# Kernel tuning notes

Hardware: AMD Instinct MI355X
Metric: run time of the kernel (lower is better)

## Reference

```python
import jax, jax.numpy as jnp
import numpy as np

H = 256       # hidden_dim
E = H // 2    # operator embedding dim
T = 12        # num_tempers
O = 3         # num_ops per temper
HOPS = 4      # max_path_hops
B = 128       # batch
D = 2048      # input_dim
NCLS = 10     # task_head classes


def setup_inputs() -> dict:
    key = jax.random.key(0)
    ks = jax.random.split(key, 12)
    x = jax.random.normal(ks[0], (B, D), jnp.float32)
    N = B * (D // H)  # 1024 patch tokens
    # per-hop routed temper per patch; value == T means halt
    sampled_tempers = jax.random.randint(ks[1], (HOPS, N), 0, T + 1, jnp.int32)
    sampled_ops = jax.random.randint(ks[2], (HOPS, N), 0, O, jnp.int32)
    s1 = 1.0 / np.sqrt(H + E)
    W1 = jax.random.uniform(ks[3], (T, O, H + E, H), jnp.float32, -s1, s1)
    b1 = jax.random.uniform(ks[4], (T, O, H), jnp.float32, -s1, s1)
    s2 = 1.0 / np.sqrt(H)
    W2 = jax.random.uniform(ks[5], (T, O, H, H), jnp.float32, -s2, s2)
    b2 = jax.random.uniform(ks[6], (T, O, H), jnp.float32, -s2, s2)
    op_emb = jax.random.normal(ks[7], (T, O, E), jnp.float32)
    ln_g = jnp.ones((H,), jnp.float32)
    ln_b = jnp.zeros((H,), jnp.float32)
    Wt = jax.random.uniform(ks[8], (H, NCLS), jnp.float32, -s2, s2)
    bt = jax.random.uniform(ks[9], (NCLS,), jnp.float32, -s2, s2)
    return dict(x=x, W1=W1, b1=b1, W2=W2, b2=b2, op_emb=op_emb,
                ln_g=ln_g, ln_b=ln_b, Wt=Wt, bt=bt,
                sampled_tempers=sampled_tempers, sampled_ops=sampled_ops)


def reference(x, W1, b1, W2, b2, op_emb, ln_g, ln_b, Wt, bt,
              sampled_tempers, sampled_ops):
    Bsz, Din = x.shape
    pad = (-Din) % H
    if pad > 0:
        x = jnp.pad(x, ((0, 0), (0, pad)))
    state = x.reshape(-1, H)                       # [N, H] patch states
    active = jnp.ones((state.shape[0],), bool)     # not-yet-halted mask
    for hop in range(HOPS):
        t = sampled_tempers[hop]
        o = sampled_ops[hop]
        active = active & (t != T)                 # T == halt action
        tc = jnp.clip(t, 0, T - 1)                 # safe index for halted rows
        emb = op_emb[tc, o]                        # [N, E] op embedding gather
        xa = jnp.concatenate([state, emb], axis=-1)  # [N, H+E]
        # per-token expert weight gather + batched matvec (memory-bound dispatch)
        h = jax.nn.relu(jnp.einsum('ni,nio->no', xa, W1[tc, o]) + b1[tc, o])
        y = jax.nn.relu(jnp.einsum('ni,nio->no', h, W2[tc, o]) + b2[tc, o])
        state = jnp.where(active[:, None], y, state)
    pooled = state.reshape(Bsz, -1, H).mean(axis=1)   # [B, H]
    mu = pooled.mean(axis=-1, keepdims=True)
    var = pooled.var(axis=-1, keepdims=True)
    normed = (pooled - mu) * jax.lax.rsqrt(var + 1e-5) * ln_g + ln_b
    return normed @ Wt + bt                           # [B, 10]
```

## Files before the change

### kernel.cpp

```cpp
#include <hip/hip_runtime.h>

typedef __attribute__((ext_vector_type(8))) short short8;
typedef __attribute__((ext_vector_type(4))) float floatx4;

#define NEXP   36
#define NTOK   1024
#define HOPS   4

#define OFF_STATE   0u
#define OFF_W1B     1048576u
#define OFF_W2B     5767168u
#define OFF_C1      10485760u
#define OFF_COUNTS  10522624u
#define OFF_LISTS   10523264u

__device__ __forceinline__ unsigned short f2bf(float f) {
    unsigned u = __float_as_uint(f);
    u += 0x7FFFu + ((u >> 16) & 1u);
    return (unsigned short)(u >> 16);
}

__global__ __launch_bounds__(256) void prep_kernel(
    const float* __restrict__ x, const float* __restrict__ W1,
    const float* __restrict__ b1, const float* __restrict__ W2,
    const float* __restrict__ op_emb,
    const int* __restrict__ tempers, const int* __restrict__ ops,
    float* __restrict__ state, unsigned short* __restrict__ W1b,
    unsigned short* __restrict__ W2b, float* __restrict__ c1,
    int* __restrict__ counts, int* __restrict__ lists)
{
    const int bid = blockIdx.x;
    const int t = threadIdx.x;

    if (bid < 2304) {
        const int mat = bid / 1152;
        const int id  = bid % 1152;
        const int e   = id / 32;
        const int sub = id % 32;
        const int kb  = sub / 4;
        const int jt  = sub % 4;
        const float* src = mat ? (W2 + e * 65536) : (W1 + e * 98304);
        unsigned short* dst = (mat ? W2b : W1b) + e * 65536;
        const int j  = jt * 64 + (t & 63);
        const int ks = (t >> 6) * 8;
        short8 v;
        #pragma unroll
        for (int i = 0; i < 8; i++)
            v[i] = (short)f2bf(src[(kb * 32 + ks + i) * 256 + j]);
        *(short8*)(dst + (kb * 256 + j) * 32 + ks) = v;
    } else if (bid < 2340) {
        const int e = bid - 2304;
        __shared__ float eb[128];
        if (t < 128) eb[t] = op_emb[e * 128 + t];
        __syncthreads();
        float acc = b1[e * 256 + t];
        const float* wp = W1 + e * 98304 + 256 * 256;
        #pragma unroll 4
        for (int k = 0; k < 128; k++)
            acc += eb[k] * wp[k * 256 + t];
        c1[e * 256 + t] = acc;
    } else if (bid < 2404) {
        const int cb = bid - 2340;
        const float4* xs = (const float4*)x;
        float4* ss = (float4*)state;
        #pragma unroll
        for (int p = 0; p < 4; p++) {
            int i4 = cb * 1024 + p * 256 + t;
            ss[i4] = xs[i4];
        }
    } else {
        __shared__ int lc[HOPS * NEXP];
        if (t < HOPS * NEXP) lc[t] = 0;
        __syncthreads();
        for (int q = 0; q < 4; q++) {
            int n = q * 256 + t;
            bool act = true;
            for (int hop = 0; hop < HOPS; hop++) {
                int tt = tempers[hop * NTOK + n];
                int oo = ops[hop * NTOK + n];
                act = act && (tt != 12);
                if (act) {
                    int e = tt * 3 + oo;
                    int pos = atomicAdd(&lc[hop * NEXP + e], 1);
                    lists[(hop * NEXP + e) * NTOK + pos] = n;
                }
            }
        }
        __syncthreads();
        if (t < HOPS * NEXP) counts[t] = lc[t];
    }
}

__global__ __launch_bounds__(1024) void hop_kernel(
    float* __restrict__ state,
    const unsigned short* __restrict__ W1b,
    const unsigned short* __restrict__ W2b,
    const float* __restrict__ c1, const float* __restrict__ b2,
    const int* __restrict__ counts, const int* __restrict__ lists, int hop)
{
    const int e   = blockIdx.x;
    const int n_e = counts[hop * NEXP + e];
    if (n_e == 0) return;

    const int t = threadIdx.x;
    const int l = t & 63, w = t >> 6;
    const int col = l & 15, g = l >> 4;
    const int j = w * 16 + col;

    const unsigned short* Wp  = W1b + e * 65536;
    const unsigned short* Wp2 = W2b + e * 65536;
    short8 B1[8], B2[8];
    #pragma unroll
    for (int kb = 0; kb < 8; kb++) {
        B1[kb] = *(const short8*)(Wp  + (kb * 256 + j) * 32 + g * 8);
        B2[kb] = *(const short8*)(Wp2 + (kb * 256 + j) * 32 + g * 8);
    }
    const float cv = c1[e * 256 + j];
    const float bv = b2[e * 256 + j];

    __shared__ int toks[16];
    __shared__ unsigned short Ab[4096];
    __shared__ unsigned short Hb[4096];

    const int* lp = lists + (hop * NEXP + e) * NTOK;

    for (int m0 = 0; m0 < n_e; m0 += 16) {
        const int mact = min(16, n_e - m0);
        __syncthreads();
        if (t < 16) toks[t] = (t < mact) ? lp[m0 + t] : 0;
        __syncthreads();

        {
            int m = t >> 6;
            int k = (t & 63) * 4;
            float4 v = make_float4(0.f, 0.f, 0.f, 0.f);
            if (m < mact) v = *(const float4*)(state + toks[m] * 256 + k);
            int kb = k >> 5, gg = (k >> 3) & 3, i = k & 7;
            unsigned short* d = Ab + kb * 512 + (gg * 16 + m) * 8 + i;
            d[0] = f2bf(v.x); d[1] = f2bf(v.y); d[2] = f2bf(v.z); d[3] = f2bf(v.w);
        }
        __syncthreads();

        floatx4 acc = (floatx4){cv, cv, cv, cv};
        #pragma unroll
        for (int kb = 0; kb < 8; kb++) {
            short8 a = *(const short8*)(Ab + kb * 512 + l * 8);
            acc = __builtin_amdgcn_mfma_f32_16x16x32_bf16(a, B1[kb], acc, 0, 0, 0);
        }
        {
            int kb2 = j >> 5, g2 = (j >> 3) & 3, i2 = j & 7;
            #pragma unroll
            for (int r = 0; r < 4; r++) {
                int m = g * 4 + r;
                float vv = acc[r];
                vv = vv > 0.f ? vv : 0.f;
                Hb[kb2 * 512 + (g2 * 16 + m) * 8 + i2] = f2bf(vv);
            }
        }
        __syncthreads();

        floatx4 acc2 = (floatx4){bv, bv, bv, bv};
        #pragma unroll
        for (int kb = 0; kb < 8; kb++) {
            short8 a = *(const short8*)(Hb + kb * 512 + l * 8);
            acc2 = __builtin_amdgcn_mfma_f32_16x16x32_bf16(a, B2[kb], acc2, 0, 0, 0);
        }
        #pragma unroll
        for (int r = 0; r < 4; r++) {
            int m = g * 4 + r;
            if (m < mact) {
                float vv = acc2[r];
                state[toks[m] * 256 + j] = vv > 0.f ? vv : 0.f;
            }
        }
    }
}

__global__ __launch_bounds__(256) void final_kernel(
    const float* __restrict__ state, const float* __restrict__ ln_g,
    const float* __restrict__ ln_b, const float* __restrict__ Wt,
    const float* __restrict__ bt, float* __restrict__ out)
{
    const int b = blockIdx.x, t = threadIdx.x;
    float s = 0.f;
    #pragma unroll
    for (int p = 0; p < 8; p++) s += state[(b * 8 + p) * 256 + t];
    s *= 0.125f;

    float v1 = s, v2 = s * s;
    #pragma unroll
    for (int off = 32; off; off >>= 1) {
        v1 += __shfl_down(v1, off);
        v2 += __shfl_down(v2, off);
    }
    __shared__ float red[8];
    __shared__ float stats[2];
    const int w = t >> 6, l = t & 63;
    if (l == 0) { red[w] = v1; red[4 + w] = v2; }
    __syncthreads();
    if (t == 0) {
        float su = red[0] + red[1] + red[2] + red[3];
        float sq = red[4] + red[5] + red[6] + red[7];
        float mu = su * (1.0f / 256.0f);
        float var = sq * (1.0f / 256.0f) - mu * mu;
        stats[0] = mu;
        stats[1] = rsqrtf(var + 1e-5f);
    }
    __syncthreads();
    float normed = (s - stats[0]) * stats[1] * ln_g[t] + ln_b[t];

    __shared__ float pr[40];
    #pragma unroll
    for (int c = 0; c < 10; c++) {
        float pv = normed * Wt[t * 10 + c];
        #pragma unroll
        for (int off = 32; off; off >>= 1) pv += __shfl_down(pv, off);
        if (l == 0) pr[w * 10 + c] = pv;
    }
    __syncthreads();
    if (t < 10)
        out[b * 10 + t] = pr[t] + pr[10 + t] + pr[20 + t] + pr[30 + t] + bt[t];
}

extern "C" void kernel_launch(void* const* d_in, const int* in_sizes, int n_in,
                              void* d_out, int out_size, void* d_ws, size_t ws_size,
                              hipStream_t stream)
{
    const float* x      = (const float*)d_in[0];
    const float* W1     = (const float*)d_in[1];
    const float* b1     = (const float*)d_in[2];
    const float* W2     = (const float*)d_in[3];
    const float* b2     = (const float*)d_in[4];
    const float* op_emb = (const float*)d_in[5];
    const float* ln_g   = (const float*)d_in[6];
    const float* ln_b   = (const float*)d_in[7];
    const float* Wt     = (const float*)d_in[8];
    const float* bt     = (const float*)d_in[9];
    const int* tempers  = (const int*)d_in[10];
    const int* ops      = (const int*)d_in[11];

    char* ws = (char*)d_ws;
    float* state          = (float*)(ws + OFF_STATE);
    unsigned short* W1b   = (unsigned short*)(ws + OFF_W1B);
    unsigned short* W2b   = (unsigned short*)(ws + OFF_W2B);
    float* c1             = (float*)(ws + OFF_C1);
    int* counts           = (int*)(ws + OFF_COUNTS);
    int* lists            = (int*)(ws + OFF_LISTS);
    float* out            = (float*)d_out;

    prep_kernel<<<2405, 256, 0, stream>>>(x, W1, b1, W2, op_emb, tempers, ops,
                                          state, W1b, W2b, c1, counts, lists);
    for (int hop = 0; hop < HOPS; hop++)
        hop_kernel<<<NEXP, 1024, 0, stream>>>(state, W1b, W2b, c1, b2,
                                              counts, lists, hop);
    final_kernel<<<128, 256, 0, stream>>>(state, ln_g, ln_b, Wt, bt, out);
}
```

Measured before the change: 146.8 us.

## Fuse all hops into one persistent kernel with per-token progress flags

Replaces the four per-hop launches, each using 36 blocks that loop over their expert's tokens, with a single launch of 256 blocks. Work is split into 16-token jobs spread across 64 slots per hop. Each token carries the hop of its last update, and a block spins on a per-token progress counter (acquire/release) before reading that token's state. This removes launch gaps and inter-hop serialization and raises parallelism, at the cost of reloading expert weights per job and the risk of spin-wait stalls or deadlock if dependent blocks are not co-resident.

```diff
diff --git a/kernel.cpp b/kernel.cpp
--- a/kernel.cpp
+++ b/kernel.cpp
@@ -13,6 +13,9 @@
 #define OFF_C1      10485760u
 #define OFF_COUNTS  10522624u
 #define OFF_LISTS   10523264u
+#define OFF_JOBS    11113088u
+#define OFF_NJ      11115136u
+#define OFF_PROG    11115152u
 
 __device__ __forceinline__ unsigned short f2bf(float f) {
     unsigned u = __float_as_uint(f);
@@ -27,7 +30,8 @@
     const int* __restrict__ tempers, const int* __restrict__ ops,
     float* __restrict__ state, unsigned short* __restrict__ W1b,
     unsigned short* __restrict__ W2b, float* __restrict__ c1,
-    int* __restrict__ counts, int* __restrict__ lists)
+    int* __restrict__ counts, int* __restrict__ lists,
+    int* __restrict__ jobs, int* __restrict__ njobs, int* __restrict__ prog)
 {
     const int bid = blockIdx.x;
     const int t = threadIdx.x;
@@ -74,7 +78,9 @@
         __syncthreads();
         for (int q = 0; q < 4; q++) {
             int n = q * 256 + t;
+            prog[n] = 0;
             bool act = true;
+            int la = 0;
             for (int hop = 0; hop < HOPS; hop++) {
                 int tt = tempers[hop * NTOK + n];
                 int oo = ops[hop * NTOK + n];
@@ -82,59 +88,83 @@
                 if (act) {
                     int e = tt * 3 + oo;
                     int pos = atomicAdd(&lc[hop * NEXP + e], 1);
-                    lists[(hop * NEXP + e) * NTOK + pos] = n;
+                    lists[(hop * NEXP + e) * NTOK + pos] = n | (la << 12);
+                    la = hop + 1;
                 }
             }
         }
         __syncthreads();
         if (t < HOPS * NEXP) counts[t] = lc[t];
-    }
-}
-
-__global__ __launch_bounds__(1024) void hop_kernel(
+        if (t < HOPS) {
+            int hop = t, nj = 0;
+            for (int e = 0; e < NEXP; e++) {
+                int c = lc[hop * NEXP + e];
+                for (int m0 = 0; m0 < c; m0 += 16)
+                    jobs[hop * 128 + nj++] = (m0 << 8) | e;
+            }
+            njobs[hop] = nj;
+        }
+    }
+}
+
+__global__ __launch_bounds__(1024) void hops_kernel(
     float* __restrict__ state,
     const unsigned short* __restrict__ W1b,
     const unsigned short* __restrict__ W2b,
     const float* __restrict__ c1, const float* __restrict__ b2,
-    const int* __restrict__ counts, const int* __restrict__ lists, int hop)
-{
-    const int e   = blockIdx.x;
-    const int n_e = counts[hop * NEXP + e];
-    if (n_e == 0) return;
+    const int* __restrict__ counts, const int* __restrict__ lists,
+    const int* __restrict__ jobs, const int* __restrict__ njobs,
+    int* __restrict__ prog)
+{
+    const int hop  = blockIdx.x >> 6;
+    const int slot = blockIdx.x & 63;
+    const int nj   = njobs[hop];
 
     const int t = threadIdx.x;
     const int l = t & 63, w = t >> 6;
     const int col = l & 15, g = l >> 4;
     const int j = w * 16 + col;
 
-    const unsigned short* Wp  = W1b + e * 65536;
-    const unsigned short* Wp2 = W2b + e * 65536;
-    short8 B1[8], B2[8];
-    #pragma unroll
-    for (int kb = 0; kb < 8; kb++) {
-        B1[kb] = *(const short8*)(Wp  + (kb * 256 + j) * 32 + g * 8);
-        B2[kb] = *(const short8*)(Wp2 + (kb * 256 + j) * 32 + g * 8);
-    }
-    const float cv = c1[e * 256 + j];
-    const float bv = b2[e * 256 + j];
-
-    __shared__ int toks[16];
+    __shared__ int tv[16];
     __shared__ unsigned short Ab[4096];
     __shared__ unsigned short Hb[4096];
 
-    const int* lp = lists + (hop * NEXP + e) * NTOK;
-
-    for (int m0 = 0; m0 < n_e; m0 += 16) {
+    for (int jb = slot; jb < nj; jb += 64) {
+        const int job = jobs[hop * 128 + jb];
+        const int e   = job & 0xFF;
+        const int m0  = job >> 8;
+        const int n_e = counts[hop * NEXP + e];
         const int mact = min(16, n_e - m0);
-        __syncthreads();
-        if (t < 16) toks[t] = (t < mact) ? lp[m0 + t] : 0;
+
+        const unsigned short* Wp  = W1b + e * 65536;
+        const unsigned short* Wp2 = W2b + e * 65536;
+        short8 B1[8], B2[8];
+        #pragma unroll
+        for (int kb = 0; kb < 8; kb++) {
+            B1[kb] = *(const short8*)(Wp  + (kb * 256 + j) * 32 + g * 8);
+            B2[kb] = *(const short8*)(Wp2 + (kb * 256 + j) * 32 + g * 8);
+        }
+        const float cv = c1[e * 256 + j];
+        const float bv = b2[e * 256 + j];
+
+        __syncthreads();
+        if (t < 16) {
+            int v = (t < mact) ? lists[(hop * NEXP + e) * NTOK + m0 + t] : 0;
+            tv[t] = v;
+            if (t < mact) {
+                int n = v & 0xFFF, need = v >> 12;
+                while (__hip_atomic_load(&prog[n], __ATOMIC_ACQUIRE,
+                                         __HIP_MEMORY_SCOPE_AGENT) < need)
+                    __builtin_amdgcn_s_sleep(1);
+            }
+        }
         __syncthreads();
 
         {
             int m = t >> 6;
             int k = (t & 63) * 4;
             float4 v = make_float4(0.f, 0.f, 0.f, 0.f);
-            if (m < mact) v = *(const float4*)(state + toks[m] * 256 + k);
+            if (m < mact) v = *(const float4*)(state + (tv[m] & 0xFFF) * 256 + k);
             int kb = k >> 5, gg = (k >> 3) & 3, i = k & 7;
             unsigned short* d = Ab + kb * 512 + (gg * 16 + m) * 8 + i;
             d[0] = f2bf(v.x); d[1] = f2bf(v.y); d[2] = f2bf(v.z); d[3] = f2bf(v.w);
@@ -170,8 +200,15 @@
             int m = g * 4 + r;
             if (m < mact) {
                 float vv = acc2[r];
-                state[toks[m] * 256 + j] = vv > 0.f ? vv : 0.f;
-            }
+                state[(tv[m] & 0xFFF) * 256 + j] = vv > 0.f ? vv : 0.f;
+            }
+        }
+
+        __syncthreads();
+        if (t < mact) {
+            __threadfence();
+            __hip_atomic_store(&prog[tv[t] & 0xFFF], hop + 1,
+                               __ATOMIC_RELEASE, __HIP_MEMORY_SCOPE_AGENT);
         }
     }
 }
@@ -246,12 +283,15 @@
     float* c1             = (float*)(ws + OFF_C1);
     int* counts           = (int*)(ws + OFF_COUNTS);
     int* lists            = (int*)(ws + OFF_LISTS);
+    int* jobs             = (int*)(ws + OFF_JOBS);
+    int* njobs            = (int*)(ws + OFF_NJ);
+    int* prog             = (int*)(ws + OFF_PROG);
     float* out            = (float*)d_out;
 
     prep_kernel<<<2405, 256, 0, stream>>>(x, W1, b1, W2, op_emb, tempers, ops,
-                                          state, W1b, W2b, c1, counts, lists);
-    for (int hop = 0; hop < HOPS; hop++)
-        hop_kernel<<<NEXP, 1024, 0, stream>>>(state, W1b, W2b, c1, b2,
-                                              counts, lists, hop);
+                                          state, W1b, W2b, c1, counts, lists,
+                                          jobs, njobs, prog);
+    hops_kernel<<<256, 1024, 0, stream>>>(state, W1b, W2b, c1, b2,
+                                          counts, lists, jobs, njobs, prog);
     final_kernel<<<128, 256, 0, stream>>>(state, ln_g, ln_b, Wt, bt, out);
 }
```

New measurement: 194.3 us. 1.32x slower.

## Split expert work into per-16-token jobs and drop state copy from x

Applied to the files above, without the earlier changes.

Prep now builds a per-hop job list with one entry per (expert, 16-token chunk). Each hop launches 128 blocks, one per job, instead of 36 blocks that loop serially over their chunks, so load balance across CUs improves. The x-to-state copy is removed: hop 0 reads x directly, and the final kernel takes rows halted at hop 0 from x. The cost is that every block reloads its expert's weight fragments, so weight traffic grows, and jobs beyond 128 per hop would be silently dropped.

```diff
diff --git a/kernel.cpp b/kernel.cpp
--- a/kernel.cpp
+++ b/kernel.cpp
@@ -13,6 +13,8 @@
 #define OFF_C1      10485760u
 #define OFF_COUNTS  10522624u
 #define OFF_LISTS   10523264u
+#define OFF_JOBS    11113088u
+#define OFF_NJ      11115136u
 
 __device__ __forceinline__ unsigned short f2bf(float f) {
     unsigned u = __float_as_uint(f);
@@ -21,13 +23,12 @@
 }
 
 __global__ __launch_bounds__(256) void prep_kernel(
-    const float* __restrict__ x, const float* __restrict__ W1,
-    const float* __restrict__ b1, const float* __restrict__ W2,
-    const float* __restrict__ op_emb,
+    const float* __restrict__ W1, const float* __restrict__ b1,
+    const float* __restrict__ W2, const float* __restrict__ op_emb,
     const int* __restrict__ tempers, const int* __restrict__ ops,
-    float* __restrict__ state, unsigned short* __restrict__ W1b,
-    unsigned short* __restrict__ W2b, float* __restrict__ c1,
-    int* __restrict__ counts, int* __restrict__ lists)
+    unsigned short* __restrict__ W1b, unsigned short* __restrict__ W2b,
+    float* __restrict__ c1, int* __restrict__ counts, int* __restrict__ lists,
+    int* __restrict__ jobs, int* __restrict__ njobs)
 {
     const int bid = blockIdx.x;
     const int t = threadIdx.x;
@@ -59,15 +60,6 @@
         for (int k = 0; k < 128; k++)
             acc += eb[k] * wp[k * 256 + t];
         c1[e * 256 + t] = acc;
-    } else if (bid < 2404) {
-        const int cb = bid - 2340;
-        const float4* xs = (const float4*)x;
-        float4* ss = (float4*)state;
-        #pragma unroll
-        for (int p = 0; p < 4; p++) {
-            int i4 = cb * 1024 + p * 256 + t;
-            ss[i4] = xs[i4];
-        }
     } else {
         __shared__ int lc[HOPS * NEXP];
         if (t < HOPS * NEXP) lc[t] = 0;
@@ -88,19 +80,32 @@
         }
         __syncthreads();
         if (t < HOPS * NEXP) counts[t] = lc[t];
-    }
-}
-
-__global__ __launch_bounds__(1024) void hop_kernel(
-    float* __restrict__ state,
+        if (t < HOPS) {
+            int hop = t, nj = 0;
+            for (int e = 0; e < NEXP; e++) {
+                int c = lc[hop * NEXP + e];
+                for (int m0 = 0; m0 < c; m0 += 16)
+                    jobs[hop * 128 + nj++] = (m0 << 8) | e;
+            }
+            njobs[hop] = nj;
+        }
+    }
+}
+
+__global__ __launch_bounds__(1024, 4) void hop_kernel(
+    const float* __restrict__ src, float* __restrict__ state,
     const unsigned short* __restrict__ W1b,
     const unsigned short* __restrict__ W2b,
     const float* __restrict__ c1, const float* __restrict__ b2,
-    const int* __restrict__ counts, const int* __restrict__ lists, int hop)
-{
-    const int e   = blockIdx.x;
+    const int* __restrict__ counts, const int* __restrict__ lists,
+    const int* __restrict__ jobs, const int* __restrict__ njobs, int hop)
+{
+    if (blockIdx.x >= njobs[hop]) return;
+    const int job = jobs[hop * 128 + blockIdx.x];
+    const int e   = job & 0xFF;
+    const int m0  = job >> 8;
     const int n_e = counts[hop * NEXP + e];
-    if (n_e == 0) return;
+    const int mact = min(16, n_e - m0);
 
     const int t = threadIdx.x;
     const int l = t & 63, w = t >> 6;
@@ -122,69 +127,69 @@
     __shared__ unsigned short Ab[4096];
     __shared__ unsigned short Hb[4096];
 
-    const int* lp = lists + (hop * NEXP + e) * NTOK;
-
-    for (int m0 = 0; m0 < n_e; m0 += 16) {
-        const int mact = min(16, n_e - m0);
-        __syncthreads();
-        if (t < 16) toks[t] = (t < mact) ? lp[m0 + t] : 0;
-        __syncthreads();
-
-        {
-            int m = t >> 6;
-            int k = (t & 63) * 4;
-            float4 v = make_float4(0.f, 0.f, 0.f, 0.f);
-            if (m < mact) v = *(const float4*)(state + toks[m] * 256 + k);
-            int kb = k >> 5, gg = (k >> 3) & 3, i = k & 7;
-            unsigned short* d = Ab + kb * 512 + (gg * 16 + m) * 8 + i;
-            d[0] = f2bf(v.x); d[1] = f2bf(v.y); d[2] = f2bf(v.z); d[3] = f2bf(v.w);
-        }
-        __syncthreads();
-
-        floatx4 acc = (floatx4){cv, cv, cv, cv};
-        #pragma unroll
-        for (int kb = 0; kb < 8; kb++) {
-            short8 a = *(const short8*)(Ab + kb * 512 + l * 8);
-            acc = __builtin_amdgcn_mfma_f32_16x16x32_bf16(a, B1[kb], acc, 0, 0, 0);
-        }
-        {
-            int kb2 = j >> 5, g2 = (j >> 3) & 3, i2 = j & 7;
-            #pragma unroll
-            for (int r = 0; r < 4; r++) {
-                int m = g * 4 + r;
-                float vv = acc[r];
-                vv = vv > 0.f ? vv : 0.f;
-                Hb[kb2 * 512 + (g2 * 16 + m) * 8 + i2] = f2bf(vv);
-            }
-        }
-        __syncthreads();
-
-        floatx4 acc2 = (floatx4){bv, bv, bv, bv};
-        #pragma unroll
-        for (int kb = 0; kb < 8; kb++) {
-            short8 a = *(const short8*)(Hb + kb * 512 + l * 8);
-            acc2 = __builtin_amdgcn_mfma_f32_16x16x32_bf16(a, B2[kb], acc2, 0, 0, 0);
-        }
+    if (t < 16) toks[t] = (t < mact) ? lists[(hop * NEXP + e) * NTOK + m0 + t] : 0;
+    __syncthreads();
+
+    {
+        int m = t >> 6;
+        int k = (t & 63) * 4;
+        float4 v = make_float4(0.f, 0.f, 0.f, 0.f);
+        if (m < mact) v = *(const float4*)(src + toks[m] * 256 + k);
+        int kb = k >> 5, gg = (k >> 3) & 3, i = k & 7;
+        unsigned short* d = Ab + kb * 512 + (gg * 16 + m) * 8 + i;
+        d[0] = f2bf(v.x); d[1] = f2bf(v.y); d[2] = f2bf(v.z); d[3] = f2bf(v.w);
+    }
+    __syncthreads();
+
+    floatx4 acc = (floatx4){cv, cv, cv, cv};
+    #pragma unroll
+    for (int kb = 0; kb < 8; kb++) {
+        short8 a = *(const short8*)(Ab + kb * 512 + l * 8);
+        acc = __builtin_amdgcn_mfma_f32_16x16x32_bf16(a, B1[kb], acc, 0, 0, 0);
+    }
+    {
+        int kb2 = j >> 5, g2 = (j >> 3) & 3, i2 = j & 7;
         #pragma unroll
         for (int r = 0; r < 4; r++) {
             int m = g * 4 + r;
-            if (m < mact) {
-                float vv = acc2[r];
-                state[toks[m] * 256 + j] = vv > 0.f ? vv : 0.f;
-            }
+            float vv = acc[r];
+            vv = vv > 0.f ? vv : 0.f;
+            Hb[kb2 * 512 + (g2 * 16 + m) * 8 + i2] = f2bf(vv);
+        }
+    }
+    __syncthreads();
+
+    floatx4 acc2 = (floatx4){bv, bv, bv, bv};
+    #pragma unroll
+    for (int kb = 0; kb < 8; kb++) {
+        short8 a = *(const short8*)(Hb + kb * 512 + l * 8);
+        acc2 = __builtin_amdgcn_mfma_f32_16x16x32_bf16(a, B2[kb], acc2, 0, 0, 0);
+    }
+    #pragma unroll
+    for (int r = 0; r < 4; r++) {
+        int m = g * 4 + r;
+        if (m < mact) {
+            float vv = acc2[r];
+            state[toks[m] * 256 + j] = vv > 0.f ? vv : 0.f;
         }
     }
 }
 
 __global__ __launch_bounds__(256) void final_kernel(
-    const float* __restrict__ state, const float* __restrict__ ln_g,
-    const float* __restrict__ ln_b, const float* __restrict__ Wt,
-    const float* __restrict__ bt, float* __restrict__ out)
+    const float* __restrict__ x, const float* __restrict__ state,
+    const int* __restrict__ tempers,
+    const float* __restrict__ ln_g, const float* __restrict__ ln_b,
+    const float* __restrict__ Wt, const float* __restrict__ bt,
+    float* __restrict__ out)
 {
     const int b = blockIdx.x, t = threadIdx.x;
     float s = 0.f;
     #pragma unroll
-    for (int p = 0; p < 8; p++) s += state[(b * 8 + p) * 256 + t];
+    for (int p = 0; p < 8; p++) {
+        int n = b * 8 + p;
+        const float* rowsrc = (tempers[n] != 12) ? state : x;
+        s += rowsrc[n * 256 + t];
+    }
     s *= 0.125f;
 
     float v1 = s, v2 = s * s;
@@ -246,12 +251,17 @@
     float* c1             = (float*)(ws + OFF_C1);
     int* counts           = (int*)(ws + OFF_COUNTS);
     int* lists            = (int*)(ws + OFF_LISTS);
+    int* jobs             = (int*)(ws + OFF_JOBS);
+    int* njobs            = (int*)(ws + OFF_NJ);
     float* out            = (float*)d_out;
 
-    prep_kernel<<<2405, 256, 0, stream>>>(x, W1, b1, W2, op_emb, tempers, ops,
-                                          state, W1b, W2b, c1, counts, lists);
+    prep_kernel<<<2341, 256, 0, stream>>>(W1, b1, W2, op_emb, tempers, ops,
+                                          W1b, W2b, c1, counts, lists,
+                                          jobs, njobs);
     for (int hop = 0; hop < HOPS; hop++)
-        hop_kernel<<<NEXP, 1024, 0, stream>>>(state, W1b, W2b, c1, b2,
-                                              counts, lists, hop);
-    final_kernel<<<128, 256, 0, stream>>>(state, ln_g, ln_b, Wt, bt, out);
-}
+        hop_kernel<<<128, 1024, 0, stream>>>(hop == 0 ? x : state, state,
+                                             W1b, W2b, c1, b2,
+                                             counts, lists, jobs, njobs, hop);
+    final_kernel<<<128, 256, 0, stream>>>(x, state, tempers,
+                                          ln_g, ln_b, Wt, bt, out);
+}
```

New measurement: 140.9 us. -4.1%, faster.
